# Performance work log

Measured on AMD Instinct MI355X. Metric: run time of the kernel, lower is better.

Reference implementation:

```python
import jax, jax.numpy as jnp
import numpy as np

# Dims (match init_kwargs / module defaults)
RD, PD = 128, 64          # residue_dim, pair_dim
H, QD, VD = 12, 32, 32    # num_heads, q_dim, v_dim
QP, VP = 8, 8             # num_q_points, num_v_points
LN_EPS = 1e-5
DIR_EPS = 1e-4
INF = 1e5


def _layer_norm(x, g, b):
    m = x.mean(-1, keepdims=True)
    v = ((x - m) ** 2).mean(-1, keepdims=True)
    return (x - m) * jax.lax.rsqrt(v + LN_EPS) * g + b


def setup_inputs() -> dict:
    key = jax.random.key(0)
    ks = jax.random.split(key, 24)
    N, L = 2, 512
    inp = {}
    inp['R'] = jax.random.normal(ks[0], (N, L, 3, 3), jnp.float32)
    inp['coord'] = jax.random.normal(ks[1], (N, L, 3), jnp.float32)
    inp['residue_feat'] = jax.random.normal(ks[2], (N, L, RD), jnp.float32)
    inp['pair_feat'] = jax.random.normal(ks[3], (N, L, L, PD), jnp.float32)
    inp['mask'] = jax.random.randint(ks[4], (N, L), 0, 2).astype(bool)

    def lin(k, fan_in, fan_out):  # torch nn.Linear default init, weight (out, in)
        lim = 1.0 / np.sqrt(fan_in)
        return jax.random.uniform(k, (fan_out, fan_in), jnp.float32, -lim, lim)

    inp['Wq'] = lin(ks[5], RD, QD * H)
    inp['Wk'] = lin(ks[6], RD, QD * H)
    inp['Wv'] = lin(ks[7], RD, VD * H)
    inp['Wpb'] = lin(ks[8], PD, H)
    inp['spatial_coef'] = jnp.full((1, 1, 1, H), np.log(np.exp(1.0) - 1.0), jnp.float32)
    inp['Wqp'] = lin(ks[9], RD, QP * H * 3)
    inp['Wkp'] = lin(ks[10], RD, QP * H * 3)
    inp['Wvp'] = lin(ks[11], RD, VP * H * 3)
    in_feat = H * VD + H * PD + H * VP * (3 + 3 + 1)  # 1824
    inp['Wout'] = lin(ks[12], in_feat, RD)
    inp['bout'] = jnp.zeros((RD,), jnp.float32)
    inp['Wm1'] = lin(ks[13], RD, RD)
    inp['bm1'] = jnp.zeros((RD,), jnp.float32)
    inp['Wm2'] = lin(ks[14], RD, RD)
    inp['bm2'] = jnp.zeros((RD,), jnp.float32)
    inp['Wm3'] = lin(ks[15], RD, RD)
    inp['bm3'] = jnp.zeros((RD,), jnp.float32)
    inp['ln1_g'] = jnp.ones((RD,), jnp.float32)
    inp['ln1_b'] = jnp.zeros((RD,), jnp.float32)
    inp['ln2_g'] = jnp.ones((RD,), jnp.float32)
    inp['ln2_b'] = jnp.zeros((RD,), jnp.float32)
    return inp


def _forward(R, coord, residue_feat, pair_feat, mask,
             Wq, Wk, Wv, Wpb, spatial_coef, Wqp, Wkp, Wvp,
             Wout, bout, Wm1, bm1, Wm2, bm2, Wm3, bm3,
             ln1_g, ln1_b, ln2_g, ln2_b):
    N, L, _ = residue_feat.shape

    def l2g(p):  # local->global: R @ p + t ; p: (N,L,M,3)
        return jnp.einsum('nlij,nlmj->nlmi', R, p) + coord[:, :, None, :]

    # --- node logits ---
    q = (residue_feat @ Wq.T).reshape(N, L, H, QD)
    k = (residue_feat @ Wk.T).reshape(N, L, H, QD)
    logits_node = jnp.einsum('nihd,njhd->nijh', q, k) * (1.0 / np.sqrt(QD))

    # --- pair logits ---
    logits_pair = pair_feat @ Wpb.T  # (N,L,L,H)

    # --- spatial logits ---
    qp = l2g((residue_feat @ Wqp.T).reshape(N, L, H * QP, 3)).reshape(N, L, H, QP * 3)
    kp = l2g((residue_feat @ Wkp.T).reshape(N, L, H * QP, 3)).reshape(N, L, H, QP * 3)
    # ||q_i - k_j||^2 = |q|^2 + |k|^2 - 2 q.k (avoids (N,L,L,H,3P) intermediate)
    qq = (qp ** 2).sum(-1)  # (N,L,H)
    kk = (kp ** 2).sum(-1)
    sum_sq = qq[:, :, None] + kk[:, None] - 2.0 * jnp.einsum('nihd,njhd->nijh', qp, kp)
    gamma = jax.nn.softplus(spatial_coef)  # (1,1,1,H)
    logits_spatial = sum_sq * (-gamma * np.sqrt(2.0 / (9.0 * QP)) / 2.0)

    logits = (logits_node + logits_pair + logits_spatial) * np.sqrt(1.0 / 3.0)

    # --- masked softmax over key axis (dim=2) ---
    mask_row = mask[:, :, None, None]            # (N,L,1,1)
    mask_pair = mask_row & mask[:, None, :, None]
    logits = jnp.where(mask_pair, logits, logits - INF)
    alpha = jax.nn.softmax(logits, axis=2)
    alpha = jnp.where(mask_row, alpha, 0.0)      # (N,L,L,H)

    # --- node aggregation ---
    v = (residue_feat @ Wv.T).reshape(N, L, H, VD)
    feat_node = jnp.einsum('nijh,njhd->nihd', alpha, v).reshape(N, L, H * VD)

    # --- pair aggregation ---
    feat_pair = jnp.einsum('nijh,nijc->nihc', alpha, pair_feat).reshape(N, L, H * PD)

    # --- spatial aggregation ---
    vp = l2g((residue_feat @ Wvp.T).reshape(N, L, H * VP, 3)).reshape(N, L, H, VP, 3)
    aggr = jnp.einsum('nijh,njhpc->nihpc', alpha, vp)  # (N,L,H,VP,3) global frame
    diff = aggr - coord[:, :, None, None, :]
    feat_points = jnp.einsum('nlji,nlhpj->nlhpi', R, diff)  # global->local: R^T (x - t)
    feat_dist = jnp.sqrt((feat_points ** 2).sum(-1))        # (N,L,H,VP)
    feat_dir = feat_points / (feat_dist[..., None] + DIR_EPS)
    feat_spatial = jnp.concatenate([
        feat_points.reshape(N, L, -1),
        feat_dist.reshape(N, L, -1),
        feat_dir.reshape(N, L, -1),
    ], axis=-1)

    feat_all = jnp.concatenate([feat_pair, feat_node, feat_spatial], axis=-1)
    feat_all = feat_all @ Wout.T + bout
    feat_all = jnp.where(mask[:, :, None], feat_all, 0.0)

    x = _layer_norm(residue_feat + feat_all, ln1_g, ln1_b)
    mlp = jax.nn.relu(jax.nn.relu(x @ Wm1.T + bm1) @ Wm2.T + bm2) @ Wm3.T + bm3
    return _layer_norm(x + mlp, ln2_g, ln2_b)


def reference(R, coord, residue_feat, pair_feat, mask,
              Wq, Wk, Wv, Wpb, spatial_coef, Wqp, Wkp, Wvp,
              Wout, bout, Wm1, bm1, Wm2, bm2, Wm3, bm3,
              ln1_g, ln1_b, ln2_g, ln2_b):
    return _forward(R, coord, residue_feat, pair_feat, mask,
                    Wq, Wk, Wv, Wpb, spatial_coef, Wqp, Wkp, Wvp,
                    Wout, bout, Wm1, bm1, Wm2, bm2, Wm3, bm3,
                    ln1_g, ln1_b, ln2_g, ln2_b)
```

## Files before the change

kernel.cpp:

```cpp
#include <hip/hip_runtime.h>
#include <hip/hip_bf16.h>

#define N_ 2
#define L_ 512
#define RD_ 128
#define PD_ 64
#define H_ 12
#define NL_ (N_*L_)
#define POUT_ 2016
#define FEAT_ 1824
#define INF_ 100000.0f
#define ISQD_ 0.17677669529663687f
#define ISQ3_ 0.5773502691896258f
#define LL_ ((size_t)L_*L_)

__global__ __launch_bounds__(256) void k_proj_gemm(
    const float* __restrict__ resf,
    const float* __restrict__ Wq, const float* __restrict__ Wk, const float* __restrict__ Wv,
    const float* __restrict__ Wqp, const float* __restrict__ Wkp, const float* __restrict__ Wvp,
    float* __restrict__ proj)
{
  const int rb = blockIdx.x * 8;
  const int ob = blockIdx.y * 128;
  const int tid = threadIdx.x;
  __shared__ float xt[8*132];
  __shared__ float wt[128*132];
  {
    int r = tid >> 5, kq = (tid & 31) * 4;
    float4 v = *(const float4*)(resf + (size_t)(rb + r)*RD_ + kq);
    xt[r*132+kq]=v.x; xt[r*132+kq+1]=v.y; xt[r*132+kq+2]=v.z; xt[r*132+kq+3]=v.w;
  }
  for (int m = 0; m < 16; ++m) {
    int idx = m*256 + tid;
    int r = idx >> 5, kq = (idx & 31) * 4;
    int o = ob + r;
    float4 v;
    if (o < 384)        v = *(const float4*)(Wq  + (size_t)o*RD_ + kq);
    else if (o < 768)   v = *(const float4*)(Wk  + (size_t)(o-384)*RD_ + kq);
    else if (o < 1152)  v = *(const float4*)(Wv  + (size_t)(o-768)*RD_ + kq);
    else if (o < 1440)  v = *(const float4*)(Wqp + (size_t)(o-1152)*RD_ + kq);
    else if (o < 1728)  v = *(const float4*)(Wkp + (size_t)(o-1440)*RD_ + kq);
    else if (o < POUT_) v = *(const float4*)(Wvp + (size_t)(o-1728)*RD_ + kq);
    else                v = make_float4(0.f,0.f,0.f,0.f);
    wt[r*132+kq]=v.x; wt[r*132+kq+1]=v.y; wt[r*132+kq+2]=v.z; wt[r*132+kq+3]=v.w;
  }
  __syncthreads();
  const int tt = tid & 7, g = tid >> 3;
  float acc0=0.f, acc1=0.f, acc2=0.f, acc3=0.f;
  #pragma unroll 4
  for (int k2 = 0; k2 < RD_; ++k2) {
    float xv = xt[tt*132 + k2];
    acc0 += xv * wt[(g     )*132 + k2];
    acc1 += xv * wt[(g + 32)*132 + k2];
    acc2 += xv * wt[(g + 64)*132 + k2];
    acc3 += xv * wt[(g + 96)*132 + k2];
  }
  float* dst = proj + (size_t)(rb + tt)*POUT_ + ob;
  if (ob + g      < POUT_) dst[g]      = acc0;
  if (ob + g + 32 < POUT_) dst[g+32]   = acc1;
  if (ob + g + 64 < POUT_) dst[g+64]   = acc2;
  if (ob + g + 96 < POUT_) dst[g+96]   = acc3;
}

__global__ __launch_bounds__(64) void k_rot(
    const float* __restrict__ R, const float* __restrict__ coord,
    const float* __restrict__ spc, const float* __restrict__ proj,
    float* __restrict__ qt, float* __restrict__ kt, float* __restrict__ vpg)
{
  const int t = blockIdx.x;
  const int n = t / L_, i = t % L_;
  const int tid = threadIdx.x;
  __shared__ float prow[POUT_];
  __shared__ float qpl[288], kpl[288], vpl[288];
  __shared__ float qqs[H_], kks[H_], coefs[H_];
  for (int m = tid; m < POUT_/4; m += 64)
    ((float4*)prow)[m] = *((const float4*)(proj + (size_t)t*POUT_) + m);
  if (tid < H_) coefs[tid] = -log1pf(expf(spc[tid])) * (1.0f/12.0f);
  __syncthreads();
  const float* Rm = R + (size_t)t*9;
  const float r00=Rm[0],r01=Rm[1],r02=Rm[2],r10=Rm[3],r11=Rm[4],r12=Rm[5],r20=Rm[6],r21=Rm[7],r22=Rm[8];
  const float cx = coord[(size_t)t*3], cy = coord[(size_t)t*3+1], cz = coord[(size_t)t*3+2];
  for (int idx = tid; idx < 288; idx += 64) {
    int mat = idx / 96, p = idx % 96;
    const float* s = prow + 1152 + mat*288 + p*3;
    float px=s[0], py=s[1], pz=s[2];
    float gx = r00*px + r01*py + r02*pz + cx;
    float gy = r10*px + r11*py + r12*pz + cy;
    float gz = r20*px + r21*py + r22*pz + cz;
    float* d = (mat==0? qpl : mat==1? kpl : vpl) + p*3;
    d[0]=gx; d[1]=gy; d[2]=gz;
  }
  __syncthreads();
  if (tid < 24) {
    int mat = tid / H_, h = tid % H_;
    const float* s = (mat==0? qpl : kpl) + h*24;
    float acc = 0.f;
    #pragma unroll
    for (int c2 = 0; c2 < 24; ++c2) acc += s[c2]*s[c2];
    (mat==0? qqs : kks)[h] = acc;
  }
  for (int m = tid; m < 72; m += 64)
    ((float4*)(vpg + (size_t)t*288))[m] = ((float4*)vpl)[m];
  __syncthreads();
  for (int idx = tid; idx < 2*H_*64; idx += 64) {
    int which = idx / 768, rem = idx % 768, h = rem >> 6, c = rem & 63;
    float val;
    if (which == 0) {
      if (c < 32)       val = prow[h*32 + c] * ISQD_;
      else if (c < 56)  val = qpl[h*24 + (c-32)] * (-2.0f * coefs[h]);
      else if (c == 56) val = coefs[h] * qqs[h];
      else if (c == 57) val = coefs[h];
      else              val = 0.f;
      qt[((size_t)(n*H_ + h)*L_ + i)*64 + c] = val;
    } else {
      if (c < 32)       val = prow[384 + h*32 + c];
      else if (c < 56)  val = kpl[h*24 + (c-32)];
      else if (c == 56) val = 1.0f;
      else if (c == 57) val = kks[h];
      else              val = 0.f;
      kt[((size_t)(n*H_ + h)*L_ + i)*64 + c] = val;
    }
  }
}

__global__ __launch_bounds__(256) void k_lgns(
    const float* __restrict__ qt, const float* __restrict__ kt,
    float* __restrict__ lgal)
{
  const int jb = blockIdx.x * 64, ib = blockIdx.y * 64, nh = blockIdx.z;
  const int tid = threadIdx.x;
  __shared__ float qs[64*65], ks[64*65];
  for (int m = 0; m < 4; ++m) {
    int idx = m*256 + tid;
    int r = idx >> 4, kq = (idx & 15) * 4;
    float4 a = *(const float4*)(qt + ((size_t)nh*L_ + ib + r)*64 + kq);
    qs[r*65+kq]=a.x; qs[r*65+kq+1]=a.y; qs[r*65+kq+2]=a.z; qs[r*65+kq+3]=a.w;
    float4 b = *(const float4*)(kt + ((size_t)nh*L_ + jb + r)*64 + kq);
    ks[r*65+kq]=b.x; ks[r*65+kq+1]=b.y; ks[r*65+kq+2]=b.z; ks[r*65+kq+3]=b.w;
  }
  __syncthreads();
  const int tx = tid & 15, ty = tid >> 4;
  const int i0 = ty*4, j0 = tx*4;
  float acc[4][4] = {};
  #pragma unroll 2
  for (int k2 = 0; k2 < 64; ++k2) {
    float qv[4], kv[4];
    #pragma unroll
    for (int d = 0; d < 4; ++d) { qv[d] = qs[(i0+d)*65 + k2]; kv[d] = ks[(j0+d)*65 + k2]; }
    #pragma unroll
    for (int a2 = 0; a2 < 4; ++a2)
      #pragma unroll
      for (int b2 = 0; b2 < 4; ++b2) acc[a2][b2] += qv[a2]*kv[b2];
  }
  #pragma unroll
  for (int a2 = 0; a2 < 4; ++a2) {
    float4 v = make_float4(acc[a2][0], acc[a2][1], acc[a2][2], acc[a2][3]);
    *(float4*)(lgal + ((size_t)nh*L_ + ib + i0 + a2)*L_ + jb + j0) = v;
  }
}

__global__ __launch_bounds__(256) void k_pbias(
    const float* __restrict__ pair, const int* __restrict__ mask,
    const float* __restrict__ Wpb, float* __restrict__ lgal)
{
  const int jt2 = blockIdx.x, i = blockIdx.y, n = blockIdx.z;
  const int bi = n*L_ + i;
  const int tid = threadIdx.x;
  __shared__ float pt[2][64*67];
  const int sr = tid >> 4, scq = (tid & 15)*4;
  #pragma unroll
  for (int m = 0; m < 4; ++m) {
    int r = m*16 + sr;
    float4 v = *(const float4*)(pair + ((size_t)bi*L_ + jt2*128 + r)*PD_ + scq);
    float* d = pt[0] + r*67 + scq;
    d[0]=v.x; d[1]=v.y; d[2]=v.z; d[3]=v.w;
  }
  __syncthreads();
  float4 rg[4];
  #pragma unroll
  for (int m = 0; m < 4; ++m) {
    int r = m*16 + sr;
    rg[m] = *(const float4*)(pair + ((size_t)bi*L_ + jt2*128 + 64 + r)*PD_ + scq);
  }

  const int r = tid & 63;
  const int w = __builtin_amdgcn_readfirstlane(tid >> 6);
  const float* w0 = Wpb + (w    )*64;
  const float* w1 = Wpb + (w + 4)*64;
  const float* w2 = Wpb + (w + 8)*64;
  const int mi = mask[bi];

  {
    const int j = jt2*128 + r;
    const float* pr = pt[0] + r*67;
    float a0=0.f, a1=0.f, a2=0.f;
    #pragma unroll 16
    for (int c = 0; c < 64; ++c) {
      float pv = pr[c];
      a0 += pv*w0[c]; a1 += pv*w1[c]; a2 += pv*w2[c];
    }
    const float mt = (mi && mask[n*L_ + j]) ? 0.f : -INF_;
    size_t base = ((size_t)(n*H_ + w)*L_ + i)*L_ + j;
    float l0 = lgal[base], l1 = lgal[base + 4*LL_], l2 = lgal[base + 8*LL_];
    lgal[base        ] = (l0 + a0)*ISQ3_ + mt;
    lgal[base + 4*LL_] = (l1 + a1)*ISQ3_ + mt;
    lgal[base + 8*LL_] = (l2 + a2)*ISQ3_ + mt;
  }

  #pragma unroll
  for (int m = 0; m < 4; ++m) {
    int rr = m*16 + sr;
    float* d = pt[1] + rr*67 + scq;
    d[0]=rg[m].x; d[1]=rg[m].y; d[2]=rg[m].z; d[3]=rg[m].w;
  }
  __syncthreads();
  {
    const int j = jt2*128 + 64 + r;
    const float* pr = pt[1] + r*67;
    float a0=0.f, a1=0.f, a2=0.f;
    #pragma unroll 16
    for (int c = 0; c < 64; ++c) {
      float pv = pr[c];
      a0 += pv*w0[c]; a1 += pv*w1[c]; a2 += pv*w2[c];
    }
    const float mt = (mi && mask[n*L_ + j]) ? 0.f : -INF_;
    size_t base = ((size_t)(n*H_ + w)*L_ + i)*L_ + j;
    float l0 = lgal[base], l1 = lgal[base + 4*LL_], l2 = lgal[base + 8*LL_];
    lgal[base        ] = (l0 + a0)*ISQ3_ + mt;
    lgal[base + 4*LL_] = (l1 + a1)*ISQ3_ + mt;
    lgal[base + 8*LL_] = (l2 + a2)*ISQ3_ + mt;
  }
}

__global__ __launch_bounds__(256) void k_softx(
    const int* __restrict__ mask, float* __restrict__ lgal)
{
  const int tid = threadIdx.x;
  const int wid = tid >> 6, lane = tid & 63;
  const int rid = blockIdx.x*4 + wid;
  const int i = rid & (L_-1);
  const int nh = rid >> 9;
  const int n = nh / H_;
  float4* r4 = (float4*)(lgal + (size_t)rid * L_);
  float4 p0 = r4[lane], p1 = r4[lane + 64];
  float mx = fmaxf(fmaxf(fmaxf(p0.x,p0.y),fmaxf(p0.z,p0.w)),
                   fmaxf(fmaxf(p1.x,p1.y),fmaxf(p1.z,p1.w)));
  #pragma unroll
  for (int off = 1; off < 64; off <<= 1) mx = fmaxf(mx, __shfl_xor(mx, off, 64));
  p0.x = expf(p0.x - mx); p0.y = expf(p0.y - mx);
  p0.z = expf(p0.z - mx); p0.w = expf(p0.w - mx);
  p1.x = expf(p1.x - mx); p1.y = expf(p1.y - mx);
  p1.z = expf(p1.z - mx); p1.w = expf(p1.w - mx);
  float s = p0.x+p0.y+p0.z+p0.w + p1.x+p1.y+p1.z+p1.w;
  #pragma unroll
  for (int off = 1; off < 64; off <<= 1) s += __shfl_xor(s, off, 64);
  const float inv = (mask[n*L_ + i] ? 1.f : 0.f) / s;
  p0.x*=inv; p0.y*=inv; p0.z*=inv; p0.w*=inv;
  p1.x*=inv; p1.y*=inv; p1.z*=inv; p1.w*=inv;
  r4[lane] = p0; r4[lane + 64] = p1;
}

__global__ __launch_bounds__(256) void k_paggr(
    const float* __restrict__ pair, const float* __restrict__ lgal,
    float* __restrict__ feat)
{
  const int i = blockIdx.x, n = blockIdx.y;
  const int bi = n*L_ + i;
  const int tid = threadIdx.x;
  const int w = tid >> 6, l = tid & 63;
  const int js = l >> 4, cq = (l & 15) << 2;
  __shared__ float part[4][H_][64];

  const float* pb = pair + ((size_t)bi*L_ + w*128 + js)*PD_ + cq;
  const float* ab[H_];
  #pragma unroll
  for (int h = 0; h < H_; ++h)
    ab[h] = lgal + ((size_t)(n*H_ + h)*L_ + i)*L_ + w*128 + js;

  float4 acc[H_];
  #pragma unroll
  for (int h = 0; h < H_; ++h) acc[h] = make_float4(0.f,0.f,0.f,0.f);

  #pragma unroll 2
  for (int g = 0; g < 32; ++g) {
    float4 pv = *(const float4*)(pb + (size_t)g*4*PD_);
    #pragma unroll
    for (int h = 0; h < H_; ++h) {
      float av = ab[h][g*4];
      acc[h].x += av*pv.x; acc[h].y += av*pv.y;
      acc[h].z += av*pv.z; acc[h].w += av*pv.w;
    }
  }

  #pragma unroll
  for (int h = 0; h < H_; ++h) {
    acc[h].x += __shfl_xor(acc[h].x, 16, 64);
    acc[h].y += __shfl_xor(acc[h].y, 16, 64);
    acc[h].z += __shfl_xor(acc[h].z, 16, 64);
    acc[h].w += __shfl_xor(acc[h].w, 16, 64);
    acc[h].x += __shfl_xor(acc[h].x, 32, 64);
    acc[h].y += __shfl_xor(acc[h].y, 32, 64);
    acc[h].z += __shfl_xor(acc[h].z, 32, 64);
    acc[h].w += __shfl_xor(acc[h].w, 32, 64);
  }
  if (l < 16) {
    #pragma unroll
    for (int h = 0; h < H_; ++h)
      *(float4*)(&part[w][h][cq]) = acc[h];
  }
  __syncthreads();
  for (int u = tid; u < H_*64; u += 256) {
    int h = u >> 6, c = u & 63;
    feat[(size_t)bi*FEAT_ + h*64 + c] =
        part[0][h][c] + part[1][h][c] + part[2][h][c] + part[3][h][c];
  }
}

__global__ __launch_bounds__(256) void k_av(
    const float* __restrict__ lgal, const float* __restrict__ proj,
    const float* __restrict__ vpg, float* __restrict__ pav)
{
  const int ib = blockIdx.x * 64;
  const int nh = blockIdx.y;
  const int z  = blockIdx.z;
  const int n = nh / H_, h = nh % H_, nL = n*L_;
  const int tid = threadIdx.x;
  __shared__ float as[64*65];
  __shared__ float bs[64*60];
  const int tx = tid & 15, ty = tid >> 4;
  const int i0 = ty*4, c0 = tx*4;
  float acc[4][4] = {};
  for (int jb = z*256; jb < z*256 + 256; jb += 64) {
    for (int m = 0; m < 4; ++m) {
      int idx = m*256 + tid;
      int r = idx >> 4, jq = (idx & 15) * 4;
      float4 a = *(const float4*)(lgal + ((size_t)nh*L_ + ib + r)*L_ + jb + jq);
      as[r*65+jq]=a.x; as[r*65+jq+1]=a.y; as[r*65+jq+2]=a.z; as[r*65+jq+3]=a.w;
    }
    for (int m = 0; m < 4; ++m) {
      int idx = m*256 + tid;
      int j = idx >> 4, qq = idx & 15;
      if (qq < 14) {
        float4 v;
        if (qq < 8) v = *(const float4*)(proj + (size_t)(nL + jb + j)*POUT_ + 768 + h*32 + qq*4);
        else        v = *(const float4*)(vpg  + (size_t)(nL + jb + j)*288  + h*24 + (qq-8)*4);
        float* d = bs + j*60 + qq*4;
        d[0]=v.x; d[1]=v.y; d[2]=v.z; d[3]=v.w;
      }
    }
    __syncthreads();
    #pragma unroll 2
    for (int k2 = 0; k2 < 64; ++k2) {
      float av[4];
      #pragma unroll
      for (int d = 0; d < 4; ++d) av[d] = as[(i0+d)*65 + k2];
      float4 bv = *(const float4*)(bs + k2*60 + c0);
      #pragma unroll
      for (int a2 = 0; a2 < 4; ++a2) {
        acc[a2][0] += av[a2]*bv.x; acc[a2][1] += av[a2]*bv.y;
        acc[a2][2] += av[a2]*bv.z; acc[a2][3] += av[a2]*bv.w;
      }
    }
    __syncthreads();
  }
  if (c0 < 56) {
    #pragma unroll
    for (int a2 = 0; a2 < 4; ++a2)
      *(float4*)(pav + (((size_t)z*24 + nh)*L_ + ib + i0 + a2)*56 + c0) =
          make_float4(acc[a2][0], acc[a2][1], acc[a2][2], acc[a2][3]);
  }
}

__global__ __launch_bounds__(256) void k_avred(
    const float* __restrict__ pav, float* __restrict__ feat,
    float* __restrict__ aggr)
{
  const int tok = blockIdx.x, tid = threadIdx.x;
  const int n = tok / L_, i = tok % L_;
  float* fb = feat + (size_t)tok*FEAT_;
  float* ag = aggr + (size_t)tok*288;
  for (int u = tid; u < 672; u += 256) {
    int h = u / 56, c = u % 56;
    size_t off = (((size_t)(n*H_ + h))*L_ + i)*56 + c;
    float v = pav[off] + pav[off + (size_t)24*L_*56];
    if (c < 32) fb[768 + h*32 + c] = v;
    else        ag[h*24 + (c - 32)] = v;
  }
}

__global__ __launch_bounds__(128) void k_post(
    const float* __restrict__ R, const float* __restrict__ coord,
    const float* __restrict__ aggr, float* __restrict__ feat)
{
  const int t = blockIdx.x, tid = threadIdx.x;
  if (tid >= 96) return;
  const float* Rm = R + (size_t)t*9;
  const float cx = coord[(size_t)t*3], cy = coord[(size_t)t*3+1], cz = coord[(size_t)t*3+2];
  const float* ag = aggr + (size_t)t*288;
  float* fb = feat + (size_t)t*FEAT_;
  float dx = ag[tid*3] - cx, dy = ag[tid*3+1] - cy, dz = ag[tid*3+2] - cz;
  float fx = Rm[0]*dx + Rm[3]*dy + Rm[6]*dz;
  float fy = Rm[1]*dx + Rm[4]*dy + Rm[7]*dz;
  float fz = Rm[2]*dx + Rm[5]*dy + Rm[8]*dz;
  float dist = sqrtf(fx*fx + fy*fy + fz*fz);
  float idn = 1.f/(dist + 1e-4f);
  fb[1152+tid*3]=fx; fb[1152+tid*3+1]=fy; fb[1152+tid*3+2]=fz;
  fb[1440+tid]=dist;
  fb[1536+tid*3]=fx*idn; fb[1536+tid*3+1]=fy*idn; fb[1536+tid*3+2]=fz*idn;
}

__global__ __launch_bounds__(256) void k_y_gemm(
    const float* __restrict__ feat, const float* __restrict__ Wout,
    float* __restrict__ ybuf)
{
  const int rb = blockIdx.x * 8;
  const int ob = blockIdx.y * 64;
  const int tid = threadIdx.x;
  __shared__ float wt[96*65];
  __shared__ float ft[96*10];
  const int o = tid & 63, tg = tid >> 6;
  float acc0 = 0.f, acc1 = 0.f;
  for (int kb = 0; kb < FEAT_; kb += 96) {
    for (int m = 0; m < 6; ++m) {
      int idx = m*256 + tid;
      int r = idx / 24, cq = (idx % 24) * 4;
      float4 v = *(const float4*)(Wout + (size_t)(ob + r)*FEAT_ + kb + cq);
      wt[(cq  )*65 + r] = v.x;
      wt[(cq+1)*65 + r] = v.y;
      wt[(cq+2)*65 + r] = v.z;
      wt[(cq+3)*65 + r] = v.w;
    }
    if (tid < 192) {
      int t = tid / 24, cq = (tid % 24) * 4;
      float4 v = *(const float4*)(feat + (size_t)(rb + t)*FEAT_ + kb + cq);
      ft[(cq  )*10 + t] = v.x;
      ft[(cq+1)*10 + t] = v.y;
      ft[(cq+2)*10 + t] = v.z;
      ft[(cq+3)*10 + t] = v.w;
    }
    __syncthreads();
    #pragma unroll 4
    for (int k2 = 0; k2 < 96; ++k2) {
      float wv = wt[k2*65 + o];
      float2 fv = *(const float2*)(ft + k2*10 + tg*2);
      acc0 += wv * fv.x;
      acc1 += wv * fv.y;
    }
    __syncthreads();
  }
  ybuf[(size_t)(rb + tg*2    )*RD_ + ob + o] = acc0;
  ybuf[(size_t)(rb + tg*2 + 1)*RD_ + ob + o] = acc1;
}

__device__ __forceinline__ float bsum128(float v, float* red, int tid) {
  #pragma unroll
  for (int off = 1; off < 64; off <<= 1) v += __shfl_xor(v, off, 64);
  __syncthreads();
  if ((tid & 63) == 0) red[tid >> 6] = v;
  __syncthreads();
  return red[0] + red[1];
}

__global__ __launch_bounds__(128) void k_mlp(
    const float* __restrict__ resf, const int* __restrict__ mask,
    const float* __restrict__ ybuf, const float* __restrict__ bout,
    const float* __restrict__ Wm1, const float* __restrict__ bm1,
    const float* __restrict__ Wm2, const float* __restrict__ bm2,
    const float* __restrict__ Wm3, const float* __restrict__ bm3,
    const float* __restrict__ g1, const float* __restrict__ b1,
    const float* __restrict__ g2, const float* __restrict__ b2,
    float* __restrict__ out)
{
  const int t = blockIdx.x, tid = threadIdx.x;
  __shared__ float xb[RD_], h1b[RD_], h2b[RD_];
  __shared__ float red[2];
  float acc = ybuf[(size_t)t*RD_ + tid] + bout[tid];
  if (mask[t] == 0) acc = 0.f;
  float r = resf[(size_t)t*RD_ + tid] + acc;

  float mean = bsum128(r, red, tid) * (1.f/RD_);
  float d = r - mean;
  float var = bsum128(d*d, red, tid) * (1.f/RD_);
  float xn = d * rsqrtf(var + 1e-5f) * g1[tid] + b1[tid];
  xb[tid] = xn;
  __syncthreads();

  float a1 = bm1[tid];
  {
    const float4* w4 = (const float4*)(Wm1 + (size_t)tid*RD_);
    #pragma unroll
    for (int c = 0; c < RD_/4; ++c) { float4 a = w4[c]; a1 += a.x*xb[4*c]+a.y*xb[4*c+1]+a.z*xb[4*c+2]+a.w*xb[4*c+3]; }
  }
  a1 = fmaxf(a1, 0.f);
  h1b[tid] = a1;
  __syncthreads();

  float a2 = bm2[tid];
  {
    const float4* w4 = (const float4*)(Wm2 + (size_t)tid*RD_);
    #pragma unroll
    for (int c = 0; c < RD_/4; ++c) { float4 a = w4[c]; a2 += a.x*h1b[4*c]+a.y*h1b[4*c+1]+a.z*h1b[4*c+2]+a.w*h1b[4*c+3]; }
  }
  a2 = fmaxf(a2, 0.f);
  h2b[tid] = a2;
  __syncthreads();

  float a3 = bm3[tid];
  {
    const float4* w4 = (const float4*)(Wm3 + (size_t)tid*RD_);
    #pragma unroll
    for (int c = 0; c < RD_/4; ++c) { float4 a = w4[c]; a3 += a.x*h2b[4*c]+a.y*h2b[4*c+1]+a.z*h2b[4*c+2]+a.w*h2b[4*c+3]; }
  }
  float r2 = xn + a3;
  float mean2 = bsum128(r2, red, tid) * (1.f/RD_);
  float d2 = r2 - mean2;
  float var2 = bsum128(d2*d2, red, tid) * (1.f/RD_);
  out[(size_t)t*RD_ + tid] = d2 * rsqrtf(var2 + 1e-5f) * g2[tid] + b2[tid];
}

extern "C" void kernel_launch(void* const* d_in, const int* in_sizes, int n_in,
                              void* d_out, int out_size, void* d_ws, size_t ws_size,
                              hipStream_t stream) {
  (void)in_sizes; (void)n_in; (void)out_size; (void)ws_size;
  const float* R     = (const float*)d_in[0];
  const float* coord = (const float*)d_in[1];
  const float* resf  = (const float*)d_in[2];
  const float* pair  = (const float*)d_in[3];
  const int*   mask  = (const int*)  d_in[4];
  const float* Wq    = (const float*)d_in[5];
  const float* Wk    = (const float*)d_in[6];
  const float* Wv    = (const float*)d_in[7];
  const float* Wpb   = (const float*)d_in[8];
  const float* spc   = (const float*)d_in[9];
  const float* Wqp   = (const float*)d_in[10];
  const float* Wkp   = (const float*)d_in[11];
  const float* Wvp   = (const float*)d_in[12];
  const float* Wout  = (const float*)d_in[13];
  const float* bout  = (const float*)d_in[14];
  const float* Wm1   = (const float*)d_in[15];
  const float* bm1   = (const float*)d_in[16];
  const float* Wm2   = (const float*)d_in[17];
  const float* bm2   = (const float*)d_in[18];
  const float* Wm3   = (const float*)d_in[19];
  const float* bm3   = (const float*)d_in[20];
  const float* g1    = (const float*)d_in[21];
  const float* b1    = (const float*)d_in[22];
  const float* g2    = (const float*)d_in[23];
  const float* b2    = (const float*)d_in[24];

  float* ws   = (float*)d_ws;
  float* proj = ws;
  float* qt   = proj + (size_t)NL_*POUT_;
  float* kt   = qt   + (size_t)N_*H_*L_*64;
  float* vpg  = kt   + (size_t)N_*H_*L_*64;
  float* lgal = vpg  + (size_t)NL_*288;
  float* feat = lgal + (size_t)N_*H_*L_*L_;
  float* ybuf = feat + (size_t)NL_*FEAT_;
  float* aggr = ybuf + (size_t)NL_*RD_;
  float* pav  = qt;

  k_proj_gemm<<<dim3(NL_/8, 16), 256, 0, stream>>>(resf, Wq, Wk, Wv, Wqp, Wkp, Wvp, proj);
  k_rot<<<NL_, 64, 0, stream>>>(R, coord, spc, proj, qt, kt, vpg);
  k_lgns<<<dim3(L_/64, L_/64, N_*H_), 256, 0, stream>>>(qt, kt, lgal);
  k_pbias<<<dim3(L_/128, L_, N_), 256, 0, stream>>>(pair, mask, Wpb, lgal);
  k_softx<<<(N_*H_*L_)/4, 256, 0, stream>>>(mask, lgal);
  k_paggr<<<dim3(L_, N_), 256, 0, stream>>>(pair, lgal, feat);
  k_av<<<dim3(L_/64, N_*H_, 2), 256, 0, stream>>>(lgal, proj, vpg, pav);
  k_avred<<<NL_, 256, 0, stream>>>(pav, feat, aggr);
  k_post<<<NL_, 128, 0, stream>>>(R, coord, aggr, feat);
  k_y_gemm<<<dim3(NL_/8, 2), 256, 0, stream>>>(feat, Wout, ybuf);
  k_mlp<<<NL_, 128, 0, stream>>>(resf, mask, ybuf, bout, Wm1, bm1, Wm2, bm2, Wm3, bm3,
                                 g1, b1, g2, b2, (float*)d_out);
}
```

Before: 244.4 us.

## Split attention-value GEMM over 8 key chunks, fuse reduce with post, vectorize LDS reads

The attention-times-value kernel now splits the key dimension into 8 chunks of 64 instead of 2 chunks of 256, so more blocks run in parallel and each block does a single load-compute pass. The partials go to a dedicated workspace region and are summed in k_avred. That kernel also absorbs the former k_post point transform through shared memory, which removes a launch and the aggr round trip. Both small GEMMs now read shared memory as float2 with a padding of 66, cutting LDS instruction count. The cost is 4x more partial-sum traffic, and the new pav region needs enough workspace after ybuf.

```diff
diff --git a/kernel.cpp b/kernel.cpp
--- a/kernel.cpp
+++ b/kernel.cpp
@@ -129,28 +129,32 @@
 {
   const int jb = blockIdx.x * 64, ib = blockIdx.y * 64, nh = blockIdx.z;
   const int tid = threadIdx.x;
-  __shared__ float qs[64*65], ks[64*65];
+  __shared__ float qs[64*66], ks[64*66];
   for (int m = 0; m < 4; ++m) {
     int idx = m*256 + tid;
     int r = idx >> 4, kq = (idx & 15) * 4;
     float4 a = *(const float4*)(qt + ((size_t)nh*L_ + ib + r)*64 + kq);
-    qs[r*65+kq]=a.x; qs[r*65+kq+1]=a.y; qs[r*65+kq+2]=a.z; qs[r*65+kq+3]=a.w;
+    qs[r*66+kq]=a.x; qs[r*66+kq+1]=a.y; qs[r*66+kq+2]=a.z; qs[r*66+kq+3]=a.w;
     float4 b = *(const float4*)(kt + ((size_t)nh*L_ + jb + r)*64 + kq);
-    ks[r*65+kq]=b.x; ks[r*65+kq+1]=b.y; ks[r*65+kq+2]=b.z; ks[r*65+kq+3]=b.w;
+    ks[r*66+kq]=b.x; ks[r*66+kq+1]=b.y; ks[r*66+kq+2]=b.z; ks[r*66+kq+3]=b.w;
   }
   __syncthreads();
   const int tx = tid & 15, ty = tid >> 4;
   const int i0 = ty*4, j0 = tx*4;
   float acc[4][4] = {};
-  #pragma unroll 2
-  for (int k2 = 0; k2 < 64; ++k2) {
-    float qv[4], kv[4];
-    #pragma unroll
-    for (int d = 0; d < 4; ++d) { qv[d] = qs[(i0+d)*65 + k2]; kv[d] = ks[(j0+d)*65 + k2]; }
+  #pragma unroll 4
+  for (int k2 = 0; k2 < 64; k2 += 2) {
+    float2 qv[4], kv[4];
+    #pragma unroll
+    for (int d = 0; d < 4; ++d) {
+      qv[d] = *(const float2*)(qs + (i0+d)*66 + k2);
+      kv[d] = *(const float2*)(ks + (j0+d)*66 + k2);
+    }
     #pragma unroll
     for (int a2 = 0; a2 < 4; ++a2)
       #pragma unroll
-      for (int b2 = 0; b2 < 4; ++b2) acc[a2][b2] += qv[a2]*kv[b2];
+      for (int b2 = 0; b2 < 4; ++b2)
+        acc[a2][b2] += qv[a2].x*kv[b2].x + qv[a2].y*kv[b2].y;
   }
   #pragma unroll
   for (int a2 = 0; a2 < 4; ++a2) {
@@ -323,45 +327,46 @@
   const int ib = blockIdx.x * 64;
   const int nh = blockIdx.y;
   const int z  = blockIdx.z;
+  const int jb = z*64;
   const int n = nh / H_, h = nh % H_, nL = n*L_;
   const int tid = threadIdx.x;
-  __shared__ float as[64*65];
+  __shared__ float as[64*66];
   __shared__ float bs[64*60];
   const int tx = tid & 15, ty = tid >> 4;
   const int i0 = ty*4, c0 = tx*4;
+  for (int m = 0; m < 4; ++m) {
+    int idx = m*256 + tid;
+    int r = idx >> 4, jq = (idx & 15) * 4;
+    float4 a = *(const float4*)(lgal + ((size_t)nh*L_ + ib + r)*L_ + jb + jq);
+    as[r*66+jq]=a.x; as[r*66+jq+1]=a.y; as[r*66+jq+2]=a.z; as[r*66+jq+3]=a.w;
+  }
+  for (int m = 0; m < 4; ++m) {
+    int idx = m*256 + tid;
+    int j = idx >> 4, qq = idx & 15;
+    if (qq < 14) {
+      float4 v;
+      if (qq < 8) v = *(const float4*)(proj + (size_t)(nL + jb + j)*POUT_ + 768 + h*32 + qq*4);
+      else        v = *(const float4*)(vpg  + (size_t)(nL + jb + j)*288  + h*24 + (qq-8)*4);
+      float* d = bs + j*60 + qq*4;
+      d[0]=v.x; d[1]=v.y; d[2]=v.z; d[3]=v.w;
+    }
+  }
+  __syncthreads();
   float acc[4][4] = {};
-  for (int jb = z*256; jb < z*256 + 256; jb += 64) {
-    for (int m = 0; m < 4; ++m) {
-      int idx = m*256 + tid;
-      int r = idx >> 4, jq = (idx & 15) * 4;
-      float4 a = *(const float4*)(lgal + ((size_t)nh*L_ + ib + r)*L_ + jb + jq);
-      as[r*65+jq]=a.x; as[r*65+jq+1]=a.y; as[r*65+jq+2]=a.z; as[r*65+jq+3]=a.w;
-    }
-    for (int m = 0; m < 4; ++m) {
-      int idx = m*256 + tid;
-      int j = idx >> 4, qq = idx & 15;
-      if (qq < 14) {
-        float4 v;
-        if (qq < 8) v = *(const float4*)(proj + (size_t)(nL + jb + j)*POUT_ + 768 + h*32 + qq*4);
-        else        v = *(const float4*)(vpg  + (size_t)(nL + jb + j)*288  + h*24 + (qq-8)*4);
-        float* d = bs + j*60 + qq*4;
-        d[0]=v.x; d[1]=v.y; d[2]=v.z; d[3]=v.w;
-      }
-    }
-    __syncthreads();
-    #pragma unroll 2
-    for (int k2 = 0; k2 < 64; ++k2) {
-      float av[4];
-      #pragma unroll
-      for (int d = 0; d < 4; ++d) av[d] = as[(i0+d)*65 + k2];
-      float4 bv = *(const float4*)(bs + k2*60 + c0);
-      #pragma unroll
-      for (int a2 = 0; a2 < 4; ++a2) {
-        acc[a2][0] += av[a2]*bv.x; acc[a2][1] += av[a2]*bv.y;
-        acc[a2][2] += av[a2]*bv.z; acc[a2][3] += av[a2]*bv.w;
-      }
-    }
-    __syncthreads();
+  #pragma unroll 4
+  for (int k2 = 0; k2 < 64; k2 += 2) {
+    float2 av[4];
+    #pragma unroll
+    for (int d = 0; d < 4; ++d) av[d] = *(const float2*)(as + (i0+d)*66 + k2);
+    float4 bv0 = *(const float4*)(bs + (k2  )*60 + c0);
+    float4 bv1 = *(const float4*)(bs + (k2+1)*60 + c0);
+    #pragma unroll
+    for (int a2 = 0; a2 < 4; ++a2) {
+      acc[a2][0] += av[a2].x*bv0.x + av[a2].y*bv1.x;
+      acc[a2][1] += av[a2].x*bv0.y + av[a2].y*bv1.y;
+      acc[a2][2] += av[a2].x*bv0.z + av[a2].y*bv1.z;
+      acc[a2][3] += av[a2].x*bv0.w + av[a2].y*bv1.w;
+    }
   }
   if (c0 < 56) {
     #pragma unroll
@@ -372,41 +377,37 @@
 }
 
 __global__ __launch_bounds__(256) void k_avred(
-    const float* __restrict__ pav, float* __restrict__ feat,
-    float* __restrict__ aggr)
+    const float* __restrict__ pav, const float* __restrict__ R,
+    const float* __restrict__ coord, float* __restrict__ feat)
 {
   const int tok = blockIdx.x, tid = threadIdx.x;
   const int n = tok / L_, i = tok % L_;
+  __shared__ float ag[288];
   float* fb = feat + (size_t)tok*FEAT_;
-  float* ag = aggr + (size_t)tok*288;
+  const size_t zstride = (size_t)24*L_*56;
   for (int u = tid; u < 672; u += 256) {
     int h = u / 56, c = u % 56;
-    size_t off = (((size_t)(n*H_ + h))*L_ + i)*56 + c;
-    float v = pav[off] + pav[off + (size_t)24*L_*56];
+    size_t base = (((size_t)(n*H_ + h))*L_ + i)*56 + c;
+    float v = 0.f;
+    #pragma unroll
+    for (int zz = 0; zz < 8; ++zz) v += pav[base + zz*zstride];
     if (c < 32) fb[768 + h*32 + c] = v;
     else        ag[h*24 + (c - 32)] = v;
   }
-}
-
-__global__ __launch_bounds__(128) void k_post(
-    const float* __restrict__ R, const float* __restrict__ coord,
-    const float* __restrict__ aggr, float* __restrict__ feat)
-{
-  const int t = blockIdx.x, tid = threadIdx.x;
-  if (tid >= 96) return;
-  const float* Rm = R + (size_t)t*9;
-  const float cx = coord[(size_t)t*3], cy = coord[(size_t)t*3+1], cz = coord[(size_t)t*3+2];
-  const float* ag = aggr + (size_t)t*288;
-  float* fb = feat + (size_t)t*FEAT_;
-  float dx = ag[tid*3] - cx, dy = ag[tid*3+1] - cy, dz = ag[tid*3+2] - cz;
-  float fx = Rm[0]*dx + Rm[3]*dy + Rm[6]*dz;
-  float fy = Rm[1]*dx + Rm[4]*dy + Rm[7]*dz;
-  float fz = Rm[2]*dx + Rm[5]*dy + Rm[8]*dz;
-  float dist = sqrtf(fx*fx + fy*fy + fz*fz);
-  float idn = 1.f/(dist + 1e-4f);
-  fb[1152+tid*3]=fx; fb[1152+tid*3+1]=fy; fb[1152+tid*3+2]=fz;
-  fb[1440+tid]=dist;
-  fb[1536+tid*3]=fx*idn; fb[1536+tid*3+1]=fy*idn; fb[1536+tid*3+2]=fz*idn;
+  __syncthreads();
+  if (tid < 96) {
+    const float* Rm = R + (size_t)tok*9;
+    const float cx = coord[(size_t)tok*3], cy = coord[(size_t)tok*3+1], cz = coord[(size_t)tok*3+2];
+    float dx = ag[tid*3] - cx, dy = ag[tid*3+1] - cy, dz = ag[tid*3+2] - cz;
+    float fx = Rm[0]*dx + Rm[3]*dy + Rm[6]*dz;
+    float fy = Rm[1]*dx + Rm[4]*dy + Rm[7]*dz;
+    float fz = Rm[2]*dx + Rm[5]*dy + Rm[8]*dz;
+    float dist = sqrtf(fx*fx + fy*fy + fz*fz);
+    float idn = 1.f/(dist + 1e-4f);
+    fb[1152+tid*3]=fx; fb[1152+tid*3+1]=fy; fb[1152+tid*3+2]=fz;
+    fb[1440+tid]=dist;
+    fb[1536+tid*3]=fx*idn; fb[1536+tid*3+1]=fy*idn; fb[1536+tid*3+2]=fz*idn;
+  }
 }
 
 __global__ __launch_bounds__(256) void k_y_gemm(
@@ -556,8 +557,7 @@
   float* lgal = vpg  + (size_t)NL_*288;
   float* feat = lgal + (size_t)N_*H_*L_*L_;
   float* ybuf = feat + (size_t)NL_*FEAT_;
-  float* aggr = ybuf + (size_t)NL_*RD_;
-  float* pav  = qt;
+  float* pav  = ybuf + (size_t)NL_*RD_;
 
   k_proj_gemm<<<dim3(NL_/8, 16), 256, 0, stream>>>(resf, Wq, Wk, Wv, Wqp, Wkp, Wvp, proj);
   k_rot<<<NL_, 64, 0, stream>>>(R, coord, spc, proj, qt, kt, vpg);
@@ -565,9 +565,8 @@
   k_pbias<<<dim3(L_/128, L_, N_), 256, 0, stream>>>(pair, mask, Wpb, lgal);
   k_softx<<<(N_*H_*L_)/4, 256, 0, stream>>>(mask, lgal);
   k_paggr<<<dim3(L_, N_), 256, 0, stream>>>(pair, lgal, feat);
-  k_av<<<dim3(L_/64, N_*H_, 2), 256, 0, stream>>>(lgal, proj, vpg, pav);
-  k_avred<<<NL_, 256, 0, stream>>>(pav, feat, aggr);
-  k_post<<<NL_, 128, 0, stream>>>(R, coord, aggr, feat);
+  k_av<<<dim3(L_/64, N_*H_, 8), 256, 0, stream>>>(lgal, proj, vpg, pav);
+  k_avred<<<NL_, 256, 0, stream>>>(pav, R, coord, feat);
   k_y_gemm<<<dim3(NL_/8, 2), 256, 0, stream>>>(feat, Wout, ybuf);
   k_mlp<<<NL_, 128, 0, stream>>>(resf, mask, ybuf, bout, Wm1, bm1, Wm2, bm2, Wm3, bm3,
                                  g1, b1, g2, b2, (float*)d_out);
```

Result: no change. 243.9 us (-0.2%).
